# Performance work log

Measured on AMD Instinct MI355X. Metric: run time of the kernel, lower is better.

Reference implementation:

```python
import jax, jax.numpy as jnp
import numpy as np

N_A = 100000   # articles
N_U = 100000   # users
E   = 1600000  # edges per edge type (avg degree 16)
D_A = 300      # article text-embedding dim
D_U = 64       # user feature dim
H   = 64       # hidden_channels
OUT = 2        # out_channels


def _lin(k, out_d, in_d, scale=0.05):
    kw, kb = jax.random.split(k)
    return (jax.random.normal(kw, (out_d, in_d)) * scale,
            jax.random.normal(kb, (out_d,)) * scale)


def setup_inputs():
    key = jax.random.key(0)
    ks = jax.random.split(key, 20)
    inp = {
        "x_article": jax.random.normal(ks[0], (N_A, D_A)),
        "x_user":    jax.random.normal(ks[1], (N_U, D_U)),
        "ei_posts":  jax.random.randint(ks[2], (2, E), 0, N_U),  # user -> article (row0 src user, row1 dst article)
        "ei_pb":     jax.random.randint(ks[3], (2, E), 0, N_A),  # article -> user
    }
    # input projections per node type
    inp["w_in_a"], inp["b_in_a"] = _lin(ks[4], H, D_A)
    inp["w_in_u"], inp["b_in_u"] = _lin(ks[5], H, D_U)
    # SAGEConv params per (layer, edge type): lin_l (with bias) on aggregated src, lin_r (no bias) on dst
    i = 6
    for layer in ("c1", "c2"):
        for et in ("p", "b"):  # p = posts (user->article), b = posted_by (article->user)
            wl, bl = _lin(ks[i], H, H); i += 1
            wr, _  = _lin(ks[i], H, H); i += 1
            inp[f"{layer}{et}_wl"] = wl
            inp[f"{layer}{et}_bl"] = bl
            inp[f"{layer}{et}_wr"] = wr
    inp["w_out"], inp["b_out"] = _lin(ks[i], OUT, H)
    return inp


def _sage(x_src, x_dst, edge_index, wl, bl, wr, n_dst):
    """PyG SAGEConv((-1,-1), H): lin_l(mean_neighbors(x_src)) + lin_r(x_dst)."""
    src, dst = edge_index[0], edge_index[1]
    msg = x_src[src]                                        # [E, H] gather
    agg = jax.ops.segment_sum(msg, dst, num_segments=n_dst)  # [n_dst, H]
    cnt = jax.ops.segment_sum(jnp.ones((edge_index.shape[1],), x_src.dtype), dst, num_segments=n_dst)
    agg = agg / jnp.maximum(cnt, 1.0)[:, None]               # mean aggregation
    return agg @ wl.T + bl + x_dst @ wr.T


def reference(x_article, x_user, ei_posts, ei_pb,
              w_in_a, b_in_a, w_in_u, b_in_u,
              c1p_wl, c1p_bl, c1p_wr, c1b_wl, c1b_bl, c1b_wr,
              c2p_wl, c2p_bl, c2p_wr, c2b_wl, c2b_bl, c2b_wr,
              w_out, b_out):
    # per-node-type input projection + ReLU
    a = jax.nn.relu(x_article @ w_in_a.T + b_in_a)  # [N_A, H]
    u = jax.nn.relu(x_user @ w_in_u.T + b_in_u)      # [N_U, H]
    # conv1 (HeteroConv mean over edge types is trivial: 1 edge type per dst type) + ReLU
    a1 = jax.nn.relu(_sage(u, a, ei_posts, c1p_wl, c1p_bl, c1p_wr, N_A))
    u1 = jax.nn.relu(_sage(a, u, ei_pb,    c1b_wl, c1b_bl, c1b_wr, N_U))
    # conv2; only the 'article' output is used by the model head
    a2 = _sage(u1, a1, ei_posts, c2p_wl, c2p_bl, c2p_wr, N_A)
    return a2 @ w_out.T + b_out  # [N_A, OUT]
```

## Files before the change

### kernel.cpp

```cpp
#include <hip/hip_runtime.h>

#define N_NODES 100000
#define EDGES   1600000
#define H 64
#define OFFPAD 100352
#define NBKT 1563
#define CHUNK 16384
#define FILL_BLKS 98

typedef unsigned int u32;
typedef unsigned short u16;
typedef short bf16x8 __attribute__((ext_vector_type(8)));
typedef float f32x4  __attribute__((ext_vector_type(4)));

__device__ __forceinline__ void bfsplit(float x, u32& h, u32& lo) {
    union { float f; u32 u; } c; c.f = x;
    u32 hu = (c.u + 0x7fffu + ((c.u >> 16) & 1u)) & 0xffff0000u;
    h = hu >> 16;
    union { u32 u; float f; } hb; hb.u = hu;
    union { float f; u32 u; } r; r.f = x - hb.f;
    lo = (r.u + 0x7fffu + ((r.u >> 16) & 1u)) >> 16;
}
__device__ __forceinline__ u16 bfrne(float x) {
    union { float f; u32 u; } c; c.f = x;
    return (u16)((c.u + 0x7fffu + ((c.u >> 16) & 1u)) >> 16);
}
__device__ __forceinline__ float bflo(u32 w)  { union { u32 u; float f; } c; c.u = w << 16; return c.f; }
__device__ __forceinline__ float bfhi(u32 w)  { union { u32 u; float f; } c; c.u = w & 0xffff0000u; return c.f; }

__global__ __launch_bounds__(256) void prep_weights(
    const float* __restrict__ w_a, const float* __restrict__ w_u,
    const float* __restrict__ b_wl, const float* __restrict__ b_wr,
    const float* __restrict__ p_wl, const float* __restrict__ p_wr,
    u32* __restrict__ pa_h, u32* __restrict__ pa_l,
    u32* __restrict__ pu_h, u32* __restrict__ pu_l,
    u32* __restrict__ pb_h, u32* __restrict__ pb_l,
    u32* __restrict__ pp_h, u32* __restrict__ pp_l)
{
    const int t = blockIdx.x * 256 + threadIdx.x;
    float v0 = 0.f, v1 = 0.f; u32* dh; u32* dl; int idx;
    if (t < 10240) {
        const int row = t / 160, u = t - row * 160, k = 2 * u;
        if (k < 300)     v0 = w_a[row * 300 + k];
        if (k + 1 < 300) v1 = w_a[row * 300 + k + 1];
        dh = pa_h; dl = pa_l; idx = t;
    } else if (t < 12288) {
        idx = t - 10240;
        const int row = idx >> 5, u = idx & 31, k = 2 * u;
        v0 = w_u[row * 64 + k]; v1 = w_u[row * 64 + k + 1];
        dh = pu_h; dl = pu_l;
    } else if (t < 16384) {
        idx = t - 12288;
        const int row = idx >> 6, u = idx & 63, k = 2 * u;
        if (k < 64) { v0 = b_wl[row * 64 + k];      v1 = b_wl[row * 64 + k + 1]; }
        else        { v0 = b_wr[row * 64 + k - 64]; v1 = b_wr[row * 64 + k - 63]; }
        dh = pb_h; dl = pb_l;
    } else {
        idx = t - 16384;
        const int row = idx >> 6, u = idx & 63, k = 2 * u;
        if (k < 64) { v0 = p_wl[row * 64 + k];      v1 = p_wl[row * 64 + k + 1]; }
        else        { v0 = p_wr[row * 64 + k - 64]; v1 = p_wr[row * 64 + k - 63]; }
        dh = pp_h; dl = pp_l;
    }
    u32 h0, l0, h1, l1; bfsplit(v0, h0, l0); bfsplit(v1, h1, l1);
    dh[idx] = h0 | (h1 << 16);
    dl[idx] = l0 | (l1 << 16);
}

template<int D, int KPAD>
__global__ __launch_bounds__(256) void proj_mfma(
    const float* __restrict__ x,
    const u32* __restrict__ wh_g, const u32* __restrict__ wl_g,
    const float* __restrict__ b, float* __restrict__ out, u16* __restrict__ outb)
{
    constexpr int NT = KPAD / 64;
    __shared__ u32 Xh[64 * 32], Xl[64 * 32], Wh[64 * 32], Wl[64 * 32];
    const int tid  = threadIdx.x;
    const int base = blockIdx.x * 64;
    const int l  = tid & 63;
    const int wv = tid >> 6;
    const int arow = wv * 16 + (l & 15);
    const int kg = l >> 4;
    f32x4 acc[4] = {};

    for (int t = 0; t < NT; ++t) {
        const int k0 = t * 64;
        for (int i = tid; i < 2048; i += 256) {
            const int row = i >> 5, u = i & 31;
            const int k = k0 + 2 * u;
            const int widx = (row << 5) | (u ^ ((row & 7) << 2));
            const int rr = min(base + row, N_NODES - 1);
            float2 v = make_float2(0.f, 0.f);
            if (k + 2 <= D) v = *(const float2*)&x[(size_t)rr * D + k];
            u32 h0, l0, h1, l1;
            bfsplit(v.x, h0, l0); bfsplit(v.y, h1, l1);
            Xh[widx] = h0 | (h1 << 16);
            Xl[widx] = l0 | (l1 << 16);
            Wh[widx] = wh_g[row * (KPAD / 2) + (k0 >> 1) + u];
            Wl[widx] = wl_g[row * (KPAD / 2) + (k0 >> 1) + u];
        }
        __syncthreads();
        #pragma unroll
        for (int s = 0; s < 2; ++s) {
            const int ka = (arow << 5) + ((s * 16 + kg * 4) ^ ((arow & 7) << 2));
            const bf16x8 ah = *(const bf16x8*)&Xh[ka];
            const bf16x8 al = *(const bf16x8*)&Xl[ka];
            #pragma unroll
            for (int c = 0; c < 4; ++c) {
                const int brow = c * 16 + (l & 15);
                const int kb = (brow << 5) + ((s * 16 + kg * 4) ^ ((brow & 7) << 2));
                const bf16x8 bh = *(const bf16x8*)&Wh[kb];
                const bf16x8 bl = *(const bf16x8*)&Wl[kb];
                acc[c] = __builtin_amdgcn_mfma_f32_16x16x32_bf16(ah, bh, acc[c], 0, 0, 0);
                acc[c] = __builtin_amdgcn_mfma_f32_16x16x32_bf16(ah, bl, acc[c], 0, 0, 0);
                acc[c] = __builtin_amdgcn_mfma_f32_16x16x32_bf16(al, bh, acc[c], 0, 0, 0);
            }
        }
        __syncthreads();
    }

    const int orow0 = base + wv * 16 + (l >> 4) * 4;
    #pragma unroll
    for (int c = 0; c < 4; ++c) {
        const int col = c * 16 + (l & 15);
        const float bv = b[col];
        #pragma unroll
        for (int i = 0; i < 4; ++i) {
            const int row = orow0 + i;
            if (row < N_NODES) {
                const float v = fmaxf(acc[c][i] + bv, 0.f);
                out[(size_t)row * H + col] = v;
                outb[(size_t)row * H + col] = bfrne(v);
            }
        }
    }
}

__global__ __launch_bounds__(256) void bucket_hist(
    const int* __restrict__ ei_p, const int* __restrict__ ei_b,
    int* __restrict__ bh_p, int* __restrict__ bh_b)
{
    __shared__ int cnt[NBKT];
    int b = blockIdx.x;
    const int* ei; int* bh;
    if (b < FILL_BLKS) { ei = ei_p; bh = bh_p; }
    else { b -= FILL_BLKS; ei = ei_b; bh = bh_b; }
    const int tid = threadIdx.x;
    for (int i = tid; i < NBKT; i += 256) cnt[i] = 0;
    __syncthreads();
    const int e0 = b * CHUNK, e1 = min(e0 + CHUNK, EDGES);
    for (int e = e0 + tid; e < e1; e += 256)
        atomicAdd(&cnt[ei[EDGES + e] >> 6], 1);
    __syncthreads();
    for (int i = tid; i < NBKT; i += 256)
        if (cnt[i]) atomicAdd(&bh[i], cnt[i]);
}

__global__ __launch_bounds__(256) void scan_nbkt(
    const int* __restrict__ bh_p, const int* __restrict__ bh_b,
    int* __restrict__ boff_p, int* __restrict__ boff_b,
    int* __restrict__ gcur_p, int* __restrict__ gcur_b)
{
    __shared__ int part[256];
    const int* bh = blockIdx.x ? bh_b : bh_p;
    int* boff = blockIdx.x ? boff_b : boff_p;
    int* gcur = blockIdx.x ? gcur_b : gcur_p;
    const int t = threadIdx.x;
    const int CH = 7;
    const int base = t * CH;
    int s = 0;
    for (int j = 0; j < CH; ++j) { int i = base + j; if (i < NBKT) s += bh[i]; }
    part[t] = s;
    __syncthreads();
    for (int d = 1; d < 256; d <<= 1) {
        int x = (t >= d) ? part[t - d] : 0;
        __syncthreads();
        part[t] += x;
        __syncthreads();
    }
    int run = part[t] - s;
    for (int j = 0; j < CH; ++j) {
        int i = base + j;
        if (i < NBKT) { boff[i] = run; gcur[i] = run; run += bh[i]; }
    }
    if (t == 0) boff[NBKT] = EDGES;
}

__global__ __launch_bounds__(256) void sort_fill(
    const int* __restrict__ ei_p, const int* __restrict__ ei_b,
    int* __restrict__ gcur_p, int* __restrict__ gcur_b,
    int* __restrict__ raw_p, int* __restrict__ raw_b)
{
    __shared__ u32 cnt[NBKT];
    __shared__ u32 base[NBKT];
    int b = blockIdx.x;
    const int* __restrict__ ei; int* __restrict__ gcur; int* __restrict__ raw;
    if (b < FILL_BLKS) { ei = ei_p; gcur = gcur_p; raw = raw_p; }
    else { b -= FILL_BLKS; ei = ei_b; gcur = gcur_b; raw = raw_b; }
    const int tid = threadIdx.x;
    const int e0 = b * CHUNK, e1 = min(e0 + CHUNK, EDGES);

    for (int i = tid; i < NBKT; i += 256) cnt[i] = 0;
    __syncthreads();
    for (int e = e0 + tid; e < e1; e += 256)
        atomicAdd(&cnt[ei[EDGES + e] >> 6], 1u);
    __syncthreads();
    for (int i = tid; i < NBKT; i += 256) {
        const u32 c = cnt[i];
        base[i] = c ? (u32)atomicAdd(&gcur[i], (int)c) : 0u;
        cnt[i] = 0;
    }
    __syncthreads();
    for (int e = e0 + tid; e < e1; e += 256) {
        const int d = ei[EDGES + e], s = ei[e];
        const int k = d >> 6;
        const u32 pos = base[k] + atomicAdd(&cnt[k], 1u);
        raw[pos] = (s << 6) | (d & 63);
    }
}

__global__ __launch_bounds__(256) void bucket_sort2(
    const int* __restrict__ raw_p, const int* __restrict__ raw_b,
    const int* __restrict__ boff_p, const int* __restrict__ boff_b,
    int* __restrict__ off_p, int* __restrict__ off_b,
    int* __restrict__ csr_p, int* __restrict__ csr_b)
{
    __shared__ int cnt[64];
    __shared__ int cur[64];
    int k = blockIdx.x;
    const int* raw; const int* boff; int* off; int* csr;
    if (k < NBKT) { raw = raw_p; boff = boff_p; off = off_p; csr = csr_p; }
    else { k -= NBKT; raw = raw_b; boff = boff_b; off = off_b; csr = csr_b; }
    const int tid = threadIdx.x;
    if (tid < 64) cnt[tid] = 0;
    __syncthreads();
    const int beg = boff[k], end = boff[k + 1];
    for (int e = beg + tid; e < end; e += 256)
        atomicAdd(&cnt[raw[e] & 63], 1);
    __syncthreads();
    if (tid == 0) {
        int run = beg;
        for (int i = 0; i < 64; ++i) { cur[i] = run; run += cnt[i]; }
    }
    __syncthreads();
    if (tid < 64) off[(k << 6) + tid] = cur[tid];
    __syncthreads();
    for (int e = beg + tid; e < end; e += 256) {
        const int id = raw[e];
        const int pos = atomicAdd(&cur[id & 63], 1);
        csr[pos] = id >> 6;
    }
}

__global__ __launch_bounds__(256) void gather_bf16(
    const u16* __restrict__ featb, const int* __restrict__ off,
    const int* __restrict__ csr, float* __restrict__ agg)
{
    const int node = (blockIdx.x * 256 + threadIdx.x) >> 6;
    const int lane = threadIdx.x & 63;
    const int grp  = lane >> 3;
    const int q    = lane & 7;
    const u32* fb = (const u32*)featb;
    const int beg = off[node], end = off[node + 1];
    float a0=0.f,a1=0.f,a2=0.f,a3=0.f,a4=0.f,a5=0.f,a6=0.f,a7=0.f;
    for (int e = beg + grp; e < end; e += 8) {
        const int s = csr[e];
        const uint4 v = *(const uint4*)&fb[((size_t)s << 5) + (q << 2)];
        a0 += bflo(v.x); a1 += bfhi(v.x);
        a2 += bflo(v.y); a3 += bfhi(v.y);
        a4 += bflo(v.z); a5 += bfhi(v.z);
        a6 += bflo(v.w); a7 += bfhi(v.w);
    }
    #pragma unroll
    for (int m = 8; m <= 32; m <<= 1) {
        a0 += __shfl_xor(a0, m, 64); a1 += __shfl_xor(a1, m, 64);
        a2 += __shfl_xor(a2, m, 64); a3 += __shfl_xor(a3, m, 64);
        a4 += __shfl_xor(a4, m, 64); a5 += __shfl_xor(a5, m, 64);
        a6 += __shfl_xor(a6, m, 64); a7 += __shfl_xor(a7, m, 64);
    }
    if (grp == 0) {
        const float inv = 1.0f / fmaxf((float)(end - beg), 1.0f);
        float4 o0 = make_float4(a0 * inv, a1 * inv, a2 * inv, a3 * inv);
        float4 o1 = make_float4(a4 * inv, a5 * inv, a6 * inv, a7 * inv);
        *(float4*)&agg[(size_t)node * H + 8 * q]     = o0;
        *(float4*)&agg[(size_t)node * H + 8 * q + 4] = o1;
    }
}

__global__ __launch_bounds__(256) void fold_head(
    const float* __restrict__ w_out, const float* __restrict__ wl2,
    const float* __restrict__ wr2, const float* __restrict__ bl2,
    const float* __restrict__ b_out, float* __restrict__ headW)
{
    const int t = threadIdx.x;
    if (t < 128) {
        int o = t >> 6, j = t & 63;
        float s = 0.f;
        for (int h = 0; h < 64; ++h) s += w_out[o * 64 + h] * wl2[h * 64 + j];
        headW[o * 64 + j] = s;
    } else {
        int idx = t - 128, o = idx >> 6, j = idx & 63;
        float s = 0.f;
        for (int h = 0; h < 64; ++h) s += w_out[o * 64 + h] * wr2[h * 64 + j];
        headW[128 + o * 64 + j] = s;
    }
    if (t < 2) {
        float s = b_out[t];
        for (int h = 0; h < 64; ++h) s += w_out[t * 64 + h] * bl2[h];
        headW[256 + t] = s;
    }
}

template<bool ZHEAD>
__global__ __launch_bounds__(256) void sage_mfma(
    const float* __restrict__ A1, const float* __restrict__ A2,
    const u32* __restrict__ wh_g, const u32* __restrict__ wl_g,
    const float* __restrict__ bias,
    const float* __restrict__ headW, float* __restrict__ z,
    float* __restrict__ outA)
{
    __shared__ u32 Ah[4096], Al[4096];
    union ShW { u32 w[4096]; float us[64 * 65]; };
    __shared__ ShW shw;
    const int tid  = threadIdx.x;
    const int base = blockIdx.x * 64;
    const int l  = tid & 63;
    const int wv = tid >> 6;
    const int arow = wv * 16 + (l & 15);
    const int kg = l >> 4;
    f32x4 acc[4] = {};

    for (int i = tid; i < 4096; i += 256) {
        const int row = i >> 6, u = i & 63;
        const int k = 2 * u;
        const int rr = min(base + row, N_NODES - 1);
        const float2 v = (k < 64)
            ? *(const float2*)&A1[(size_t)rr * H + k]
            : *(const float2*)&A2[(size_t)rr * H + (k - 64)];
        u32 h0, l0, h1, l1;
        bfsplit(v.x, h0, l0); bfsplit(v.y, h1, l1);
        const int widx = (row << 6) | (u ^ ((row & 7) << 2));
        Ah[widx] = h0 | (h1 << 16);
        Al[widx] = l0 | (l1 << 16);
    }

    #pragma unroll
    for (int t = 0; t < 2; ++t) {
        for (int i = tid; i < 2048; i += 256) {
            const int row = i >> 5, u = i & 31;
            const int widx = (row << 5) | (u ^ ((row & 7) << 2));
            shw.w[widx]        = wh_g[row * 64 + t * 32 + u];
            shw.w[2048 + widx] = wl_g[row * 64 + t * 32 + u];
        }
        __syncthreads();
        #pragma unroll
        for (int s = 0; s < 2; ++s) {
            const int ka = (arow << 6) + ((t * 32 + s * 16 + kg * 4) ^ ((arow & 7) << 2));
            const bf16x8 ah = *(const bf16x8*)&Ah[ka];
            const bf16x8 al = *(const bf16x8*)&Al[ka];
            #pragma unroll
            for (int c = 0; c < 4; ++c) {
                const int brow = c * 16 + (l & 15);
                const int kb = (brow << 5) + ((s * 16 + kg * 4) ^ ((brow & 7) << 2));
                const bf16x8 bh = *(const bf16x8*)&shw.w[kb];
                const bf16x8 bl = *(const bf16x8*)&shw.w[2048 + kb];
                acc[c] = __builtin_amdgcn_mfma_f32_16x16x32_bf16(ah, bh, acc[c], 0, 0, 0);
                acc[c] = __builtin_amdgcn_mfma_f32_16x16x32_bf16(ah, bl, acc[c], 0, 0, 0);
                acc[c] = __builtin_amdgcn_mfma_f32_16x16x32_bf16(al, bh, acc[c], 0, 0, 0);
            }
        }
        __syncthreads();
    }

    const int r0 = wv * 16 + (l >> 4) * 4;
    if (!ZHEAD) {
        #pragma unroll
        for (int c = 0; c < 4; ++c) {
            const int col = c * 16 + (l & 15);
            const float bv = bias[col];
            #pragma unroll
            for (int i = 0; i < 4; ++i) {
                const int row = base + r0 + i;
                if (row < N_NODES)
                    outA[(size_t)row * H + col] = fmaxf(acc[c][i] + bv, 0.f);
            }
        }
    } else {
        #pragma unroll
        for (int c = 0; c < 4; ++c) {
            const int col = c * 16 + (l & 15);
            const float bv = bias[col];
            #pragma unroll
            for (int i = 0; i < 4; ++i)
                shw.us[(r0 + i) * 65 + col] = fmaxf(acc[c][i] + bv, 0.f);
        }
        __syncthreads();
        if (tid < 128) {
            const int r = tid & 63, o = tid >> 6;
            const int row = base + r;
            if (row < N_NODES) {
                float v = 0.f;
                for (int k = 0; k < 64; ++k)
                    v += shw.us[r * 65 + k] * headW[o * 64 + k];
                z[(size_t)row * 2 + o] = v;
            }
        }
    }
}

__global__ __launch_bounds__(256) void final_head(
    const int* __restrict__ off, const int* __restrict__ csr,
    const float* __restrict__ z, const float* __restrict__ a1,
    const float* __restrict__ headW, float* __restrict__ out)
{
    const int node = (blockIdx.x * 256 + threadIdx.x) >> 6;
    const int lane = threadIdx.x & 63;
    const int beg = off[node], end = off[node + 1];
    float z0 = 0.f, z1 = 0.f;
    for (int e = beg + lane; e < end; e += 64) {
        int s = csr[e];
        const float2 zv = *(const float2*)&z[(size_t)s * 2];
        z0 += zv.x; z1 += zv.y;
    }
    const float av = a1[(size_t)node * H + lane];
    float p0 = av * headW[128 + lane];
    float p1 = av * headW[192 + lane];
    #pragma unroll
    for (int m = 1; m <= 32; m <<= 1) {
        z0 += __shfl_xor(z0, m, 64);
        z1 += __shfl_xor(z1, m, 64);
        p0 += __shfl_xor(p0, m, 64);
        p1 += __shfl_xor(p1, m, 64);
    }
    if (lane == 0) {
        const float inv = 1.0f / fmaxf((float)(end - beg), 1.0f);
        float2 o;
        o.x = z0 * inv + p0 + headW[256];
        o.y = z1 * inv + p1 + headW[257];
        *(float2*)&out[(size_t)node * 2] = o;
    }
}

extern "C" void kernel_launch(void* const* d_in, const int* in_sizes, int n_in,
                              void* d_out, int out_size, void* d_ws, size_t ws_size,
                              hipStream_t stream) {
    const float* x_a    = (const float*)d_in[0];
    const float* x_u    = (const float*)d_in[1];
    const int*   ei_p   = (const int*)d_in[2];
    const int*   ei_b   = (const int*)d_in[3];
    const float* w_in_a = (const float*)d_in[4];
    const float* b_in_a = (const float*)d_in[5];
    const float* w_in_u = (const float*)d_in[6];
    const float* b_in_u = (const float*)d_in[7];
    const float* c1p_wl = (const float*)d_in[8];
    const float* c1p_bl = (const float*)d_in[9];
    const float* c1p_wr = (const float*)d_in[10];
    const float* c1b_wl = (const float*)d_in[11];
    const float* c1b_bl = (const float*)d_in[12];
    const float* c1b_wr = (const float*)d_in[13];
    const float* c2p_wl = (const float*)d_in[14];
    const float* c2p_bl = (const float*)d_in[15];
    const float* c2p_wr = (const float*)d_in[16];
    const float* w_out  = (const float*)d_in[20];
    const float* b_out  = (const float*)d_in[21];

    const size_t NF = (size_t)N_NODES * H;
    float* bufA  = (float*)d_ws;
    float* bufU  = bufA + NF;
    float* agg   = bufU + NF;
    u16*   fAb   = (u16*)(agg + NF);
    u16*   fUb   = fAb + NF;
    float* z     = (float*)(fUb + NF);
    float* headW = z + 2 * N_NODES;
    int* bh_p   = (int*)(headW + 512);
    int* bh_b   = bh_p + 2048;
    int* boff_p = bh_b + 2048;
    int* boff_b = boff_p + 2048;
    int* gcur_p = boff_b + 2048;
    int* gcur_b = gcur_p + 2048;
    int* off_p  = gcur_b + 2048;
    int* off_b  = off_p + OFFPAD;
    int* csr_p  = off_b + OFFPAD;
    int* csr_b  = csr_p + EDGES;
    u32* pa_h   = (u32*)(csr_b + EDGES);
    u32* pa_l   = pa_h + 10240;
    u32* pu_h   = pa_l + 10240;
    u32* pu_l   = pu_h + 2048;
    u32* pb_h   = pu_l + 2048;
    u32* pb_l   = pb_h + 4096;
    u32* pp_h   = pb_l + 4096;
    u32* pp_l   = pp_h + 4096;
    int* raw_p  = (int*)agg;
    int* raw_b  = raw_p + EDGES;

    const dim3 blk(256);
    const int grid_gemm = (N_NODES + 63) / 64;

    prep_weights<<<80, blk, 0, stream>>>(
        w_in_a, w_in_u, c1b_wl, c1b_wr, c1p_wl, c1p_wr,
        pa_h, pa_l, pu_h, pu_l, pb_h, pb_l, pp_h, pp_l);
    fold_head<<<1, blk, 0, stream>>>(w_out, c2p_wl, c2p_wr, c2p_bl, b_out, headW);

    hipMemsetAsync(bh_p, 0, 2 * 2048 * sizeof(int), stream);
    bucket_hist<<<2 * FILL_BLKS, blk, 0, stream>>>(ei_p, ei_b, bh_p, bh_b);
    scan_nbkt<<<2, blk, 0, stream>>>(bh_p, bh_b, boff_p, boff_b, gcur_p, gcur_b);
    sort_fill<<<2 * FILL_BLKS, blk, 0, stream>>>(ei_p, ei_b, gcur_p, gcur_b, raw_p, raw_b);
    bucket_sort2<<<2 * NBKT, blk, 0, stream>>>(
        raw_p, raw_b, boff_p, boff_b, off_p, off_b, csr_p, csr_b);

    proj_mfma<300, 320><<<grid_gemm, blk, 0, stream>>>(x_a, pa_h, pa_l, b_in_a, bufA, fAb);
    proj_mfma<64, 64>  <<<grid_gemm, blk, 0, stream>>>(x_u, pu_h, pu_l, b_in_u, bufU, fUb);

    gather_bf16<<<25000, blk, 0, stream>>>(fAb, off_b, csr_b, agg);
    sage_mfma<true><<<grid_gemm, blk, 0, stream>>>(
        agg, bufU, pb_h, pb_l, c1b_bl, headW, z, nullptr);

    gather_bf16<<<25000, blk, 0, stream>>>(fUb, off_p, csr_p, agg);
    sage_mfma<false><<<grid_gemm, blk, 0, stream>>>(
        agg, bufA, pp_h, pp_l, c1p_bl, headW, nullptr, bufA);

    final_head<<<25000, blk, 0, stream>>>(off_p, csr_p, z, bufA, headW, (float*)d_out);

    (void)in_sizes; (void)n_in; (void)out_size; (void)ws_size;
}
```

Measured before the change: 388.2 us.

## Restructure CSR build into chunk-local bucket sort and widen projection loads

Replaces the global histogram, scan and atomic-cursor scatter with a per-chunk local bucket sort whose offsets are recorded per chunk. This removes the memset, the separate histogram pass and the global atomics. A second pass merges per-chunk segments into 256-node buckets. The projection GEMM staging now loads float4 and uint2 instead of float2 and u32, halving the load iterations. The risk is that the second pass reads each chunk segment serially per thread (one thread per chunk), which may give poor memory parallelism and load imbalance.

```diff
diff --git a/kernel.cpp b/kernel.cpp
--- a/kernel.cpp
+++ b/kernel.cpp
@@ -4,9 +4,10 @@
 #define EDGES   1600000
 #define H 64
 #define OFFPAD 100352
-#define NBKT 1563
-#define CHUNK 16384
-#define FILL_BLKS 98
+#define NB2 391
+#define CHUNK 8192
+#define NCHUNK 196
+#define LOSTRIDE 392
 
 typedef unsigned int u32;
 typedef unsigned short u16;
@@ -85,19 +86,30 @@
 
     for (int t = 0; t < NT; ++t) {
         const int k0 = t * 64;
-        for (int i = tid; i < 2048; i += 256) {
-            const int row = i >> 5, u = i & 31;
-            const int k = k0 + 2 * u;
+        for (int i = tid; i < 1024; i += 256) {
+            const int row = i >> 4, j = i & 15;
+            const int k = k0 + 4 * j;
+            const int u = 2 * j;
             const int widx = (row << 5) | (u ^ ((row & 7) << 2));
             const int rr = min(base + row, N_NODES - 1);
-            float2 v = make_float2(0.f, 0.f);
-            if (k + 2 <= D) v = *(const float2*)&x[(size_t)rr * D + k];
-            u32 h0, l0, h1, l1;
+            float4 v = make_float4(0.f, 0.f, 0.f, 0.f);
+            if (k + 4 <= D) {
+                v = *(const float4*)&x[(size_t)rr * D + k];
+            } else {
+                const float* xr = &x[(size_t)rr * D];
+                if (k     < D) v.x = xr[k];
+                if (k + 1 < D) v.y = xr[k + 1];
+                if (k + 2 < D) v.z = xr[k + 2];
+                if (k + 3 < D) v.w = xr[k + 3];
+            }
+            u32 h0, l0, h1, l1, h2, l2, h3, l3;
             bfsplit(v.x, h0, l0); bfsplit(v.y, h1, l1);
-            Xh[widx] = h0 | (h1 << 16);
-            Xl[widx] = l0 | (l1 << 16);
-            Wh[widx] = wh_g[row * (KPAD / 2) + (k0 >> 1) + u];
-            Wl[widx] = wl_g[row * (KPAD / 2) + (k0 >> 1) + u];
+            bfsplit(v.z, h2, l2); bfsplit(v.w, h3, l3);
+            *(uint2*)&Xh[widx] = make_uint2(h0 | (h1 << 16), h2 | (h3 << 16));
+            *(uint2*)&Xl[widx] = make_uint2(l0 | (l1 << 16), l2 | (l3 << 16));
+            const int wo = row * (KPAD / 2) + (k0 >> 1) + u;
+            *(uint2*)&Wh[widx] = *(const uint2*)&wh_g[wo];
+            *(uint2*)&Wl[widx] = *(const uint2*)&wl_g[wo];
         }
         __syncthreads();
         #pragma unroll
@@ -136,119 +148,111 @@
     }
 }
 
-__global__ __launch_bounds__(256) void bucket_hist(
-    const int* __restrict__ ei_p, const int* __restrict__ ei_b,
-    int* __restrict__ bh_p, int* __restrict__ bh_b)
-{
-    __shared__ int cnt[NBKT];
-    int b = blockIdx.x;
-    const int* ei; int* bh;
-    if (b < FILL_BLKS) { ei = ei_p; bh = bh_p; }
-    else { b -= FILL_BLKS; ei = ei_b; bh = bh_b; }
-    const int tid = threadIdx.x;
-    for (int i = tid; i < NBKT; i += 256) cnt[i] = 0;
-    __syncthreads();
-    const int e0 = b * CHUNK, e1 = min(e0 + CHUNK, EDGES);
-    for (int e = e0 + tid; e < e1; e += 256)
-        atomicAdd(&cnt[ei[EDGES + e] >> 6], 1);
-    __syncthreads();
-    for (int i = tid; i < NBKT; i += 256)
-        if (cnt[i]) atomicAdd(&bh[i], cnt[i]);
-}
-
-__global__ __launch_bounds__(256) void scan_nbkt(
-    const int* __restrict__ bh_p, const int* __restrict__ bh_b,
-    int* __restrict__ boff_p, int* __restrict__ boff_b,
-    int* __restrict__ gcur_p, int* __restrict__ gcur_b)
-{
-    __shared__ int part[256];
-    const int* bh = blockIdx.x ? bh_b : bh_p;
-    int* boff = blockIdx.x ? boff_b : boff_p;
-    int* gcur = blockIdx.x ? gcur_b : gcur_p;
-    const int t = threadIdx.x;
-    const int CH = 7;
-    const int base = t * CH;
-    int s = 0;
-    for (int j = 0; j < CH; ++j) { int i = base + j; if (i < NBKT) s += bh[i]; }
-    part[t] = s;
-    __syncthreads();
-    for (int d = 1; d < 256; d <<= 1) {
-        int x = (t >= d) ? part[t - d] : 0;
-        __syncthreads();
-        part[t] += x;
-        __syncthreads();
-    }
-    int run = part[t] - s;
-    for (int j = 0; j < CH; ++j) {
-        int i = base + j;
-        if (i < NBKT) { boff[i] = run; gcur[i] = run; run += bh[i]; }
-    }
-    if (t == 0) boff[NBKT] = EDGES;
-}
-
 __global__ __launch_bounds__(256) void sort_fill(
     const int* __restrict__ ei_p, const int* __restrict__ ei_b,
-    int* __restrict__ gcur_p, int* __restrict__ gcur_b,
+    int* __restrict__ lo_p, int* __restrict__ lo_b,
     int* __restrict__ raw_p, int* __restrict__ raw_b)
 {
-    __shared__ u32 cnt[NBKT];
-    __shared__ u32 base[NBKT];
+    __shared__ int cnt[NB2];
+    __shared__ int loc[NB2 + 1];
     int b = blockIdx.x;
-    const int* __restrict__ ei; int* __restrict__ gcur; int* __restrict__ raw;
-    if (b < FILL_BLKS) { ei = ei_p; gcur = gcur_p; raw = raw_p; }
-    else { b -= FILL_BLKS; ei = ei_b; gcur = gcur_b; raw = raw_b; }
+    const int* __restrict__ ei; int* __restrict__ lo; int* __restrict__ raw;
+    if (b < NCHUNK) { ei = ei_p; lo = lo_p; raw = raw_p; }
+    else { b -= NCHUNK; ei = ei_b; lo = lo_b; raw = raw_b; }
     const int tid = threadIdx.x;
     const int e0 = b * CHUNK, e1 = min(e0 + CHUNK, EDGES);
 
-    for (int i = tid; i < NBKT; i += 256) cnt[i] = 0;
+    for (int i = tid; i < NB2; i += 256) cnt[i] = 0;
     __syncthreads();
     for (int e = e0 + tid; e < e1; e += 256)
-        atomicAdd(&cnt[ei[EDGES + e] >> 6], 1u);
-    __syncthreads();
-    for (int i = tid; i < NBKT; i += 256) {
-        const u32 c = cnt[i];
-        base[i] = c ? (u32)atomicAdd(&gcur[i], (int)c) : 0u;
-        cnt[i] = 0;
-    }
+        atomicAdd(&cnt[ei[EDGES + e] >> 8], 1);
+    __syncthreads();
+    if (tid == 0) {
+        int run = 0;
+        for (int i = 0; i < NB2; ++i) { loc[i] = run; run += cnt[i]; }
+        loc[NB2] = run;
+    }
+    __syncthreads();
+    for (int i = tid; i <= NB2; i += 256) lo[b * LOSTRIDE + i] = loc[i];
+    for (int i = tid; i < NB2; i += 256) cnt[i] = loc[i];
     __syncthreads();
     for (int e = e0 + tid; e < e1; e += 256) {
         const int d = ei[EDGES + e], s = ei[e];
-        const int k = d >> 6;
-        const u32 pos = base[k] + atomicAdd(&cnt[k], 1u);
-        raw[pos] = (s << 6) | (d & 63);
+        const int pos = atomicAdd(&cnt[d >> 8], 1);
+        raw[e0 + pos] = (s << 8) | (d & 255);
+    }
+}
+
+__global__ __launch_bounds__(256) void scan_boff(
+    const int* __restrict__ lo_p, const int* __restrict__ lo_b,
+    int* __restrict__ boff_p, int* __restrict__ boff_b,
+    int* __restrict__ off_p, int* __restrict__ off_b)
+{
+    __shared__ int sz[NB2];
+    const int* lo = blockIdx.x ? lo_b : lo_p;
+    int* boff = blockIdx.x ? boff_b : boff_p;
+    int* off  = blockIdx.x ? off_b : off_p;
+    const int t = threadIdx.x;
+    for (int i = t; i < NB2; i += 256) sz[i] = 0;
+    __syncthreads();
+    for (int i = t; i < NCHUNK * NB2; i += 256) {
+        const int b = i / NB2, k = i - b * NB2;
+        const int v = lo[b * LOSTRIDE + k + 1] - lo[b * LOSTRIDE + k];
+        if (v) atomicAdd(&sz[k], v);
+    }
+    __syncthreads();
+    if (t == 0) {
+        int run = 0;
+        for (int k = 0; k < NB2; ++k) { boff[k] = run; run += sz[k]; }
+        boff[NB2] = EDGES;
+        off[N_NODES] = EDGES;
     }
 }
 
 __global__ __launch_bounds__(256) void bucket_sort2(
     const int* __restrict__ raw_p, const int* __restrict__ raw_b,
+    const int* __restrict__ lo_p, const int* __restrict__ lo_b,
     const int* __restrict__ boff_p, const int* __restrict__ boff_b,
     int* __restrict__ off_p, int* __restrict__ off_b,
     int* __restrict__ csr_p, int* __restrict__ csr_b)
 {
-    __shared__ int cnt[64];
-    __shared__ int cur[64];
+    __shared__ int cnt[256];
+    __shared__ int cur[256];
+    __shared__ int sb[NCHUNK], se[NCHUNK];
     int k = blockIdx.x;
-    const int* raw; const int* boff; int* off; int* csr;
-    if (k < NBKT) { raw = raw_p; boff = boff_p; off = off_p; csr = csr_p; }
-    else { k -= NBKT; raw = raw_b; boff = boff_b; off = off_b; csr = csr_b; }
+    const int* raw; const int* lo; const int* boff; int* off; int* csr;
+    if (k < NB2) { raw = raw_p; lo = lo_p; boff = boff_p; off = off_p; csr = csr_p; }
+    else { k -= NB2; raw = raw_b; lo = lo_b; boff = boff_b; off = off_b; csr = csr_b; }
     const int tid = threadIdx.x;
-    if (tid < 64) cnt[tid] = 0;
-    __syncthreads();
-    const int beg = boff[k], end = boff[k + 1];
-    for (int e = beg + tid; e < end; e += 256)
-        atomicAdd(&cnt[raw[e] & 63], 1);
+    cnt[tid] = 0;
+    if (tid < NCHUNK) {
+        sb[tid] = lo[tid * LOSTRIDE + k];
+        se[tid] = lo[tid * LOSTRIDE + k + 1];
+    }
+    __syncthreads();
+    if (tid < NCHUNK) {
+        const int base = tid * CHUNK;
+        for (int e = sb[tid]; e < se[tid]; ++e)
+            atomicAdd(&cnt[raw[base + e] & 255], 1);
+    }
     __syncthreads();
     if (tid == 0) {
-        int run = beg;
-        for (int i = 0; i < 64; ++i) { cur[i] = run; run += cnt[i]; }
-    }
-    __syncthreads();
-    if (tid < 64) off[(k << 6) + tid] = cur[tid];
-    __syncthreads();
-    for (int e = beg + tid; e < end; e += 256) {
-        const int id = raw[e];
-        const int pos = atomicAdd(&cur[id & 63], 1);
-        csr[pos] = id >> 6;
+        int run = boff[k];
+        for (int i = 0; i < 256; ++i) { cur[i] = run; run += cnt[i]; }
+    }
+    __syncthreads();
+    {
+        const int node = (k << 8) + tid;
+        if (node < N_NODES) off[node] = cur[tid];
+    }
+    __syncthreads();
+    if (tid < NCHUNK) {
+        const int base = tid * CHUNK;
+        for (int e = sb[tid]; e < se[tid]; ++e) {
+            const int id = raw[base + e];
+            const int pos = atomicAdd(&cur[id & 255], 1);
+            csr[pos] = id >> 8;
+        }
     }
 }
 
@@ -472,13 +476,11 @@
     u16*   fUb   = fAb + NF;
     float* z     = (float*)(fUb + NF);
     float* headW = z + 2 * N_NODES;
-    int* bh_p   = (int*)(headW + 512);
-    int* bh_b   = bh_p + 2048;
-    int* boff_p = bh_b + 2048;
-    int* boff_b = boff_p + 2048;
-    int* gcur_p = boff_b + 2048;
-    int* gcur_b = gcur_p + 2048;
-    int* off_p  = gcur_b + 2048;
+    int* lo_p   = (int*)(headW + 512);
+    int* lo_b   = lo_p + 77056;
+    int* boff_p = lo_b + 77056;
+    int* boff_b = boff_p + 512;
+    int* off_p  = boff_b + 512;
     int* off_b  = off_p + OFFPAD;
     int* csr_p  = off_b + OFFPAD;
     int* csr_b  = csr_p + EDGES;
@@ -501,12 +503,10 @@
         pa_h, pa_l, pu_h, pu_l, pb_h, pb_l, pp_h, pp_l);
     fold_head<<<1, blk, 0, stream>>>(w_out, c2p_wl, c2p_wr, c2p_bl, b_out, headW);
 
-    hipMemsetAsync(bh_p, 0, 2 * 2048 * sizeof(int), stream);
-    bucket_hist<<<2 * FILL_BLKS, blk, 0, stream>>>(ei_p, ei_b, bh_p, bh_b);
-    scan_nbkt<<<2, blk, 0, stream>>>(bh_p, bh_b, boff_p, boff_b, gcur_p, gcur_b);
-    sort_fill<<<2 * FILL_BLKS, blk, 0, stream>>>(ei_p, ei_b, gcur_p, gcur_b, raw_p, raw_b);
-    bucket_sort2<<<2 * NBKT, blk, 0, stream>>>(
-        raw_p, raw_b, boff_p, boff_b, off_p, off_b, csr_p, csr_b);
+    sort_fill<<<2 * NCHUNK, blk, 0, stream>>>(ei_p, ei_b, lo_p, lo_b, raw_p, raw_b);
+    scan_boff<<<2, blk, 0, stream>>>(lo_p, lo_b, boff_p, boff_b, off_p, off_b);
+    bucket_sort2<<<2 * NB2, blk, 0, stream>>>(
+        raw_p, raw_b, lo_p, lo_b, boff_p, boff_b, off_p, off_b, csr_p, csr_b);
 
     proj_mfma<300, 320><<<grid_gemm, blk, 0, stream>>>(x_a, pa_h, pa_l, b_in_a, bufA, fAb);
     proj_mfma<64, 64>  <<<grid_gemm, blk, 0, stream>>>(x_u, pu_h, pu_l, b_in_u, bufU, fUb);
```

Measured after the change: 489.9 us. 26.2% more time.
